# Kernel tuning notes

Measured on AMD Instinct MI355X. Metric: run time of the kernel, lower is better.

Reference implementation:

```python
import jax, jax.numpy as jnp
import numpy as np

N_NODES = 100000
N_EDGES = 1600000
D = 32
K = 3  # Chebyshev kernels
NEG_SLOPE = 0.2


def setup_inputs() -> dict:
    key = jax.random.key(0)
    ks = jax.random.split(key, 10)
    s = 1.0 / np.sqrt(D)
    return {
        "u": jax.random.normal(ks[0], (N_NODES, D), jnp.float32),
        "lambda_max": jnp.full((1,), 2.0, jnp.float32),
        "edge_src": jax.random.randint(ks[1], (N_EDGES,), 0, N_NODES, jnp.int32),
        "edge_dst": jax.random.randint(ks[2], (N_EDGES,), 0, N_NODES, jnp.int32),
        "cheb_W": jax.random.normal(ks[3], (K * D, D), jnp.float32) * s,
        "cheb_b": jnp.zeros((D,), jnp.float32),
        "src_W": jax.random.normal(ks[4], (D, D), jnp.float32) * s,
        "src_b": jnp.zeros((D,), jnp.float32),
        "dst_W": jax.random.normal(ks[5], (D, D), jnp.float32) * s,
        "dst_b": jnp.zeros((D,), jnp.float32),
        "attn": jax.random.normal(ks[6], (1, D), jnp.float32) * s,  # (heads=1, D)
    }


def reference(u, lambda_max, edge_src, edge_dst, cheb_W, cheb_b,
              src_W, src_b, dst_W, dst_b, attn):
    N = u.shape[0]
    # in-degrees (DGL: clamp(min=1) ** -0.5)
    deg = jnp.zeros((N,), u.dtype).at[edge_dst].add(1.0)
    Dinv = jnp.clip(deg, 1.0, None) ** -0.5  # (N,)

    def unnL(x):  # D^{-1/2} A D^{-1/2} x  via copy_u->sum message passing
        m = (x * Dinv[:, None])[edge_src]                       # (E, D)
        agg = jax.ops.segment_sum(m, edge_dst, num_segments=N)  # (N, D)
        return agg * Dinv[:, None]

    # --- ChebConv ---
    re_norm = 2.0 / lambda_max  # (1,) broadcast over all nodes
    X0 = u
    Xt = [X0]
    X1 = X0
    if K > 1:
        h = unnL(X0)
        X1 = -re_norm * h + X0 * (re_norm - 1.0)
        Xt.append(X1)
    for _ in range(2, K):
        h = unnL(X1)
        Xi = -2.0 * re_norm * h + X1 * (2.0 * (re_norm - 1.0)) - X0
        Xt.append(Xi)
        X0, X1 = X1, Xi
    Xcat = jnp.concatenate(Xt, axis=1)                 # (N, K*D)
    hc = jax.nn.relu(Xcat @ cheb_W + cheb_b)           # (N, D), DGL default activation=relu

    # --- GATv2Conv (heads=1) ---
    H = attn.shape[0]
    fsrc = (hc @ src_W + src_b).reshape(N, H, -1)      # (N, H, D)
    fdst = (hc @ dst_W + dst_b).reshape(N, H, -1)
    e = jax.nn.leaky_relu(fsrc[edge_src] + fdst[edge_dst], NEG_SLOPE)  # (E, H, D)
    logits = jnp.einsum('ehd,hd->eh', e, attn)         # (E, H)
    mx = jax.ops.segment_max(logits, edge_dst, num_segments=N)
    mx = jnp.where(jnp.isfinite(mx), mx, 0.0)
    ex = jnp.exp(logits - mx[edge_dst])
    den = jax.ops.segment_sum(ex, edge_dst, num_segments=N)
    a = ex / jnp.where(den > 0, den, 1.0)[edge_dst]    # edge softmax over dst groups
    msg = fsrc[edge_src] * a[:, :, None]               # (E, H, D)
    out = jax.ops.segment_sum(msg, edge_dst, num_segments=N)  # (N, H, D)
    return out.squeeze(1)
```

## Files before the change

kernel.cpp:

```cpp
#include <hip/hip_runtime.h>
#include <hip/hip_bf16.h>


typedef unsigned short u16;

#define DD 32
#define NEG_SLOPE 0.2f
#define BLK 256
#define TILE 4096
#define CB_SHIFT 8
#define CB_NODES 256
#define SRC_BITS 17

#define OFF_CHEBW 0
#define OFF_CHEBB 3072
#define OFF_SRCW  3104
#define OFF_SRCB  4128
#define OFF_DSTW  4160
#define OFF_DSTB  5184
#define OFF_ATTN  5216
#define OFF_LMAX  5248
#define W_TOTAL   5249

#define F_U     0
#define F_CHEBW 1
#define F_CHEBB 2
#define F_SRCW  3
#define F_SRCB  4
#define F_DSTW  5
#define F_DSTB  6
#define F_ATTN  7
#define F_LMAX  8
#define N_FLAGS 9

__device__ __forceinline__ float bh2f(u16 h) {
    return __uint_as_float(((unsigned)h) << 16);
}
__device__ __forceinline__ float rdin(const void* p, long long i, int f32f) {
    return f32f ? ((const float*)p)[i] : bh2f(((const u16*)p)[i]);
}
__device__ __forceinline__ float4 rd4(const void* p, long long row, int q, int f32f) {
    if (f32f) return ((const float4*)p)[row * 8 + q];
    ushort4 h = ((const ushort4*)p)[row * 8 + q];
    return make_float4(bh2f(h.x), bh2f(h.y), bh2f(h.z), bh2f(h.w));
}
__device__ __forceinline__ float lrelu(float x) { return fmaxf(x, NEG_SLOPE * x); }

__device__ __forceinline__ int plaus(u16 h) {
    if ((h & 0x7FFFu) == 0) return 1;
    unsigned e = (h >> 7) & 0xFF;
    return (e >= 0x60 && e <= 0x8F) ? 1 : 0;
}

template<int G>
__device__ __forceinline__ float4 bc8(float4 v) {
    constexpr int imm = (G << 5) | 0x18;
    float4 r;
    r.x = __int_as_float(__builtin_amdgcn_ds_swizzle(__float_as_int(v.x), imm));
    r.y = __int_as_float(__builtin_amdgcn_ds_swizzle(__float_as_int(v.y), imm));
    r.z = __int_as_float(__builtin_amdgcn_ds_swizzle(__float_as_int(v.z), imm));
    r.w = __int_as_float(__builtin_amdgcn_ds_swizzle(__float_as_int(v.w), imm));
    return r;
}

#define FMA4(ACC, S, W) \
    ACC.x = fmaf((S), (W).x, ACC.x); ACC.y = fmaf((S), (W).y, ACC.y); \
    ACC.z = fmaf((S), (W).z, ACC.z); ACC.w = fmaf((S), (W).w, ACC.w)

__global__ __launch_bounds__(BLK) void k_prep(
        const void* u, const void* chebW, const void* chebB, const void* srcW,
        const void* srcB, const void* dstW, const void* dstB, const void* attn,
        const void* lmax, int n0, int n7, int* __restrict__ flags,
        float* __restrict__ wsW, unsigned* __restrict__ Mabs,
        unsigned* __restrict__ gcnt) {
    __shared__ int cEven, cEvenZ, cOddNZ, fl;
    const void* ptrs[N_FLAGS] = {u, chebW, chebB, srcW, srcB, dstW, dstB, attn, lmax};
    const int   ns[N_FLAGS]   = {n0, 3072, 32, 1024, 32, 1024, 32, n7, 1};
    const int   offs[N_FLAGS] = {0, OFF_CHEBW, OFF_CHEBB, OFF_SRCW, OFF_SRCB,
                                 OFF_DSTW, OFF_DSTB, OFF_ATTN, OFF_LMAX};
    int a = blockIdx.x;
    if (a >= N_FLAGS) return;
    int t = threadIdx.x;
    const u16* h = (const u16*)ptrs[a];
    int n = ns[a];
    if (t == 0) { cEven = 0; cEvenZ = 0; cOddNZ = 0; }
    if (a == 0) {
        if (t < 32) Mabs[t] = 0u;
        if (t == 32) *gcnt = 0u;
    }
    __syncthreads();
    if (n == 1) {
        if (t == 0) {
            u16 v = h[0];
            fl = ((v & 0x7FFFu) == 0 || !plaus(v)) ? 1 : 0;
            flags[a] = fl;
        }
    } else {
        int nprobe = n >> 1;
        if (nprobe > 64) nprobe = 64;
        if (t < nprobe) {
            u16 ev = h[2 * t];
            u16 od = h[2 * t + 1];
            if (plaus(ev)) atomicAdd(&cEven, 1);
            if ((ev & 0x7FFFu) == 0) atomicAdd(&cEvenZ, 1);
            if (plaus(od) && (od & 0x7FFFu) != 0) atomicAdd(&cOddNZ, 1);
        }
        __syncthreads();
        if (t == 0) {
            int bf = (cEven * 4 >= nprobe * 3);
            if (cEvenZ == nprobe && cOddNZ * 2 >= nprobe) bf = 0;
            fl = bf ? 0 : 1;
            flags[a] = fl;
        }
    }
    __syncthreads();
    if (a == 0) return;
    int f = fl;
    int cnt = ns[a];
    int doff = offs[a];
    for (int i = t; i < cnt; i += BLK)
        wsW[doff + i] = rdin(ptrs[a], i, f);
}


__global__ __launch_bounds__(BLK) void k_h1(
        const int* __restrict__ dst, unsigned* __restrict__ hist1,
        int E, int T, int NB1) {
    __shared__ unsigned lh[512];
    int tile = blockIdx.x, t = threadIdx.x;
    for (int b = t; b < 512; b += BLK) lh[b] = 0;
    __syncthreads();
    int base = tile * TILE;
    for (int i = 0; i < TILE / BLK; i++) {
        int e = base + i * BLK + t;
        if (e < E) atomicAdd(&lh[dst[e] >> CB_SHIFT], 1u);
    }
    __syncthreads();
    for (int b = t; b < NB1; b += BLK) hist1[(size_t)b * T + tile] = lh[b];
}

__global__ __launch_bounds__(BLK) void k_scA(
        unsigned* __restrict__ h, unsigned* __restrict__ bsum, int T,
        unsigned* __restrict__ row_ptr, int N, int E,
        unsigned* __restrict__ gcnt) {
    __shared__ unsigned s[BLK];
    __shared__ int lastdone;
    int b = blockIdx.x, t = threadIdx.x;
    int NB = gridDim.x;
    unsigned carry = 0;
    for (int base = 0; base < T; base += BLK) {
        int i = base + t;
        unsigned v = (i < T) ? h[(size_t)b * T + i] : 0u;
        s[t] = v;
        __syncthreads();
        for (int off = 1; off < BLK; off <<= 1) {
            unsigned a = (t >= off) ? s[t - off] : 0u;
            __syncthreads();
            s[t] += a;
            __syncthreads();
        }
        if (i < T) h[(size_t)b * T + i] = carry + s[t] - v;
        carry += s[BLK - 1];
        __syncthreads();
    }
    if (t == 0) {
        bsum[b] = carry;
        __threadfence();
        unsigned old = atomicAdd(gcnt, 1u);
        lastdone = (old == (unsigned)(NB - 1)) ? 1 : 0;
    }
    __syncthreads();
    if (!lastdone) return;
    __threadfence();
    unsigned c2 = 0;
    for (int base = 0; base < NB; base += BLK) {
        int i = base + t;
        unsigned v = (i < NB) ? bsum[i] : 0u;
        s[t] = v;
        __syncthreads();
        for (int off = 1; off < BLK; off <<= 1) {
            unsigned a = (t >= off) ? s[t - off] : 0u;
            __syncthreads();
            s[t] += a;
            __syncthreads();
        }
        if (i < NB) bsum[i] = c2 + s[t] - v;
        c2 += s[BLK - 1];
        __syncthreads();
    }
    if (t == 0) row_ptr[N] = (unsigned)E;
}

__global__ __launch_bounds__(BLK) void k_s1(
        const int* __restrict__ src, const int* __restrict__ dst,
        const unsigned* __restrict__ off1, const unsigned* __restrict__ bsum,
        unsigned* __restrict__ tmp, int E, int T, int NB1) {
    __shared__ unsigned cur[512];
    int tile = blockIdx.x, t = threadIdx.x;
    for (int b = t; b < NB1; b += BLK)
        cur[b] = off1[(size_t)b * T + tile] + bsum[b];
    __syncthreads();
    int base = tile * TILE;
    for (int i = 0; i < TILE / BLK; i++) {
        int e = base + i * BLK + t;
        if (e < E) {
            int d = dst[e];
            unsigned pos = atomicAdd(&cur[d >> CB_SHIFT], 1u);
            tmp[pos] = ((unsigned)(d & (CB_NODES - 1)) << SRC_BITS) | (unsigned)src[e];
        }
    }
}

__global__ __launch_bounds__(BLK) void k_p2(
        const unsigned* __restrict__ tmp, const unsigned* __restrict__ bsum,
        unsigned* __restrict__ row_ptr, float* __restrict__ dinv,
        int* __restrict__ srcs, int N, int E, int T, int NB1) {
    __shared__ unsigned hist[CB_NODES], cur[CB_NODES], ssc[BLK];
    int b = blockIdx.x, t = threadIdx.x;
    int nodeBase = b << CB_SHIFT;
    unsigned lo = bsum[b];
    unsigned hi = (b + 1 < NB1) ? bsum[b + 1] : (unsigned)E;
    hist[t] = 0;
    __syncthreads();
    for (unsigned e = lo + t; e < hi; e += BLK)
        atomicAdd(&hist[tmp[e] >> SRC_BITS], 1u);
    __syncthreads();
    unsigned v = hist[t];
    ssc[t] = v;
    __syncthreads();
    for (int off = 1; off < BLK; off <<= 1) {
        unsigned a = (t >= off) ? ssc[t - off] : 0u;
        __syncthreads();
        ssc[t] += a;
        __syncthreads();
    }
    unsigned ex = ssc[t] - v;
    cur[t] = ex;
    int node = nodeBase + t;
    if (node < N) {
        row_ptr[node] = lo + ex;
        unsigned c = v;
        if (c < 1u) c = 1u;
        dinv[node] = rsqrtf((float)c);
    }
    __syncthreads();
    for (unsigned e = lo + t; e < hi; e += BLK) {
        unsigned p = tmp[e];
        unsigned pos = lo + atomicAdd(&cur[p >> SRC_BITS], 1u);
        srcs[pos] = (int)(p & ((1u << SRC_BITS) - 1u));
    }
}


__global__ __launch_bounds__(BLK) void k_unnl1(
        const void* __restrict__ u, const int* __restrict__ flags,
        const float* __restrict__ dinv, const unsigned* __restrict__ row_ptr,
        const int* __restrict__ srcs, const float* __restrict__ wsW,
        float* __restrict__ X1, int N) {
    int node = (blockIdx.x * BLK + threadIdx.x) >> 3;
    if (node >= N) return;
    int q = threadIdx.x & 7;
    int f = flags[F_U];
    int base = (int)row_ptr[node], end = (int)row_ptr[node + 1];
    float4 acc = make_float4(0.f, 0.f, 0.f, 0.f);
    for (int i = base; i < end; i += 4) {
        int e1 = i + 1, e2 = i + 2, e3 = i + 3;
        int s0 = srcs[i];
        int s1 = srcs[min(e1, end - 1)];
        int s2 = srcs[min(e2, end - 1)];
        int s3 = srcs[min(e3, end - 1)];
        float dv0 = dinv[s0], dv1 = dinv[s1], dv2 = dinv[s2], dv3 = dinv[s3];
        if (e1 >= end) dv1 = 0.f;
        if (e2 >= end) dv2 = 0.f;
        if (e3 >= end) dv3 = 0.f;
        float4 x0 = rd4(u, s0, q, f);
        float4 x1 = rd4(u, s1, q, f);
        float4 x2 = rd4(u, s2, q, f);
        float4 x3 = rd4(u, s3, q, f);
        acc.x += x0.x * dv0 + x1.x * dv1 + x2.x * dv2 + x3.x * dv3;
        acc.y += x0.y * dv0 + x1.y * dv1 + x2.y * dv2 + x3.y * dv3;
        acc.z += x0.z * dv0 + x1.z * dv1 + x2.z * dv2 + x3.z * dv3;
        acc.w += x0.w * dv0 + x1.w * dv1 + x2.w * dv2 + x3.w * dv3;
    }
    float rn = 2.0f / wsW[OFF_LMAX];
    float dn = dinv[node];
    float4 x0 = rd4(u, node, q, f);
    float4 r;
    r.x = -rn * (acc.x * dn) + x0.x * (rn - 1.f);
    r.y = -rn * (acc.y * dn) + x0.y * (rn - 1.f);
    r.z = -rn * (acc.z * dn) + x0.z * (rn - 1.f);
    r.w = -rn * (acc.w * dn) + x0.w * (rn - 1.f);
    ((float4*)X1)[(size_t)node * 8 + q] = r;
}

__global__ __launch_bounds__(BLK) void k_unnl2(
        const void* __restrict__ u, const int* __restrict__ flags,
        const float* __restrict__ X1, const float* __restrict__ dinv,
        const unsigned* __restrict__ row_ptr, const int* __restrict__ srcs,
        const float* __restrict__ wsW, float* __restrict__ X2, int N) {
    int node = (blockIdx.x * BLK + threadIdx.x) >> 3;
    if (node >= N) return;
    int q = threadIdx.x & 7;
    int base = (int)row_ptr[node], end = (int)row_ptr[node + 1];
    float4 acc = make_float4(0.f, 0.f, 0.f, 0.f);
    for (int i = base; i < end; i += 4) {
        int e1 = i + 1, e2 = i + 2, e3 = i + 3;
        int s0 = srcs[i];
        int s1 = srcs[min(e1, end - 1)];
        int s2 = srcs[min(e2, end - 1)];
        int s3 = srcs[min(e3, end - 1)];
        float dv0 = dinv[s0], dv1 = dinv[s1], dv2 = dinv[s2], dv3 = dinv[s3];
        if (e1 >= end) dv1 = 0.f;
        if (e2 >= end) dv2 = 0.f;
        if (e3 >= end) dv3 = 0.f;
        float4 x0 = ((const float4*)X1)[(size_t)s0 * 8 + q];
        float4 x1 = ((const float4*)X1)[(size_t)s1 * 8 + q];
        float4 x2 = ((const float4*)X1)[(size_t)s2 * 8 + q];
        float4 x3 = ((const float4*)X1)[(size_t)s3 * 8 + q];
        acc.x += x0.x * dv0 + x1.x * dv1 + x2.x * dv2 + x3.x * dv3;
        acc.y += x0.y * dv0 + x1.y * dv1 + x2.y * dv2 + x3.y * dv3;
        acc.z += x0.z * dv0 + x1.z * dv1 + x2.z * dv2 + x3.z * dv3;
        acc.w += x0.w * dv0 + x1.w * dv1 + x2.w * dv2 + x3.w * dv3;
    }
    float rn = 2.0f / wsW[OFF_LMAX];
    float dn = dinv[node];
    float4 x0 = rd4(u, node, q, flags[F_U]);
    float4 x1 = ((const float4*)X1)[(size_t)node * 8 + q];
    float4 r;
    r.x = -2.f * rn * (acc.x * dn) + x1.x * (2.f * (rn - 1.f)) - x0.x;
    r.y = -2.f * rn * (acc.y * dn) + x1.y * (2.f * (rn - 1.f)) - x0.y;
    r.z = -2.f * rn * (acc.z * dn) + x1.z * (2.f * (rn - 1.f)) - x0.z;
    r.w = -2.f * rn * (acc.w * dn) + x1.w * (2.f * (rn - 1.f)) - x0.w;
    ((float4*)X2)[(size_t)node * 8 + q] = r;
}

__global__ __launch_bounds__(BLK, 4) void k_cfsd(
        const void* __restrict__ u, const int* __restrict__ flags,
        const float* __restrict__ X1, const float* __restrict__ X2,
        const float* __restrict__ wsW, float* __restrict__ fsrc,
        float* __restrict__ fdst, unsigned* __restrict__ Mabs, int N) {
    __shared__ __align__(16) float sW[3072], sWs[1024], sWd[1024];
    __shared__ __align__(16) float sb[32], sbs[32], sbd[32];
    __shared__ unsigned mloc[32];
    int t = threadIdx.x;
    for (int i = t; i < 3072; i += BLK) sW[i] = wsW[OFF_CHEBW + i];
    for (int i = t; i < 1024; i += BLK) {
        sWs[i] = wsW[OFF_SRCW + i];
        sWd[i] = wsW[OFF_DSTW + i];
    }
    if (t < 32) {
        sb[t]  = wsW[OFF_CHEBB + t];
        sbs[t] = wsW[OFF_SRCB + t];
        sbd[t] = wsW[OFF_DSTB + t];
        mloc[t] = 0u;
    }
    __syncthreads();
    int f = flags[F_U];
    int q = t & 7;
    long long node = (long long)((blockIdx.x * BLK + t) >> 3);
    bool valid = node < N;
    long long row = valid ? node : (N - 1);

    const float4* fW = (const float4*)sW;
    float4 acc = ((const float4*)sb)[q];

#define CHEB_STEP(XQ, B4, I4) { \
    float4 xv = bc8<I4>(XQ); \
    const float4* wp = fW + (B4) + (I4) * 32 + q; \
    float4 w; \
    w = wp[0];  FMA4(acc, xv.x, w); \
    w = wp[8];  FMA4(acc, xv.y, w); \
    w = wp[16]; FMA4(acc, xv.z, w); \
    w = wp[24]; FMA4(acc, xv.w, w); }
#define CHEB8(XQ, B4) \
    CHEB_STEP(XQ, B4, 0) CHEB_STEP(XQ, B4, 1) CHEB_STEP(XQ, B4, 2) \
    CHEB_STEP(XQ, B4, 3) CHEB_STEP(XQ, B4, 4) CHEB_STEP(XQ, B4, 5) \
    CHEB_STEP(XQ, B4, 6) CHEB_STEP(XQ, B4, 7)

    {
        float4 xq = rd4(u, row, q, f);
        CHEB8(xq, 0)
    }
    {
        float4 xq = ((const float4*)X1)[row * 8 + q];
        CHEB8(xq, 256)
    }
    {
        float4 xq = ((const float4*)X2)[row * 8 + q];
        CHEB8(xq, 512)
    }
#undef CHEB8
#undef CHEB_STEP

    acc.x = fmaxf(acc.x, 0.f); acc.y = fmaxf(acc.y, 0.f);
    acc.z = fmaxf(acc.z, 0.f); acc.w = fmaxf(acc.w, 0.f);

    const float4* fWs = (const float4*)sWs;
    const float4* fWd = (const float4*)sWd;
    float4 as = ((const float4*)sbs)[q];
    float4 ad = ((const float4*)sbd)[q];
#define PROJ_G(G) { \
    float4 h = bc8<G>(acc); \
    const float4* wsp = fWs + (4 * (G)) * 8 + q; \
    const float4* wdp = fWd + (4 * (G)) * 8 + q; \
    float4 w; \
    w = wsp[0];  FMA4(as, h.x, w); \
    w = wsp[8];  FMA4(as, h.y, w); \
    w = wsp[16]; FMA4(as, h.z, w); \
    w = wsp[24]; FMA4(as, h.w, w); \
    w = wdp[0];  FMA4(ad, h.x, w); \
    w = wdp[8];  FMA4(ad, h.y, w); \
    w = wdp[16]; FMA4(ad, h.z, w); \
    w = wdp[24]; FMA4(ad, h.w, w); }
    PROJ_G(0) PROJ_G(1) PROJ_G(2) PROJ_G(3)
    PROJ_G(4) PROJ_G(5) PROJ_G(6) PROJ_G(7)
#undef PROJ_G

    float mabs = 0.f;
    if (valid) {
        ((float4*)fsrc)[row * 8 + q] = as;
        ((float4*)fdst)[row * 8 + q] = ad;
        mabs = fmaxf(fmaxf(fabsf(as.x), fabsf(as.y)),
                     fmaxf(fabsf(as.z), fabsf(as.w)));
    }
    atomicMax(&mloc[t & 31], __float_as_uint(mabs));
    __syncthreads();
    if (t < 32) atomicMax(&Mabs[t], mloc[t]);
}

__global__ __launch_bounds__(BLK) void k_gat(
        const float* __restrict__ fsrc, const float* __restrict__ fdst,
        const unsigned* __restrict__ row_ptr, const int* __restrict__ srcs,
        const float* __restrict__ wsW, const unsigned* __restrict__ Mabs,
        float* __restrict__ out, int N) {
    int node = (blockIdx.x * BLK + threadIdx.x) >> 3;
    if (node >= N) return;
    int q = threadIdx.x & 7;
    int base = (int)row_ptr[node], end = (int)row_ptr[node + 1];
    if (base == end) {
        ((float4*)out)[(size_t)node * 8 + q] = make_float4(0.f, 0.f, 0.f, 0.f);
        return;
    }
    float4 fd = ((const float4*)fdst)[(size_t)node * 8 + q];
    float4 at = ((const float4*)(wsW + OFF_ATTN))[q];
    float4 mb = ((const float4*)Mabs)[q];
    float kp = (mb.x + fabsf(fd.x)) * fabsf(at.x) +
               (mb.y + fabsf(fd.y)) * fabsf(at.y) +
               (mb.z + fabsf(fd.z)) * fabsf(at.z) +
               (mb.w + fabsf(fd.w)) * fabsf(at.w);
    kp += __shfl_xor(kp, 1);
    kp += __shfl_xor(kp, 2);
    kp += __shfl_xor(kp, 4);
    float K = kp;
    float4 acc = make_float4(0.f, 0.f, 0.f, 0.f);
    float den = 0.f;
    for (int i = base; i < end; i += 2) {
        int e1 = i + 1;
        int s0 = srcs[i];
        int s1 = srcs[min(e1, end - 1)];
        float4 fs0 = ((const float4*)fsrc)[(size_t)s0 * 8 + q];
        float4 fs1 = ((const float4*)fsrc)[(size_t)s1 * 8 + q];
        float v0 = lrelu(fs0.x + fd.x) * at.x + lrelu(fs0.y + fd.y) * at.y +
                   lrelu(fs0.z + fd.z) * at.z + lrelu(fs0.w + fd.w) * at.w;
        float v1 = lrelu(fs1.x + fd.x) * at.x + lrelu(fs1.y + fd.y) * at.y +
                   lrelu(fs1.z + fd.z) * at.z + lrelu(fs1.w + fd.w) * at.w;
        v0 += __shfl_xor(v0, 1);  v1 += __shfl_xor(v1, 1);
        v0 += __shfl_xor(v0, 2);  v1 += __shfl_xor(v1, 2);
        v0 += __shfl_xor(v0, 4);  v1 += __shfl_xor(v1, 4);
        float w0 = __expf(v0 - K);
        float w1 = (e1 < end) ? __expf(v1 - K) : 0.f;
        acc.x += fs0.x * w0 + fs1.x * w1;
        acc.y += fs0.y * w0 + fs1.y * w1;
        acc.z += fs0.z * w0 + fs1.z * w1;
        acc.w += fs0.w * w0 + fs1.w * w1;
        den += w0 + w1;
    }
    float inv = 1.f / (den > 0.f ? den : 1.f);
    ((float4*)out)[(size_t)node * 8 + q] =
        make_float4(acc.x * inv, acc.y * inv, acc.z * inv, acc.w * inv);
}

extern "C" void kernel_launch(void* const* d_in, const int* in_sizes, int n_in,
                              void* d_out, int out_size, void* d_ws, size_t ws_size,
                              hipStream_t stream) {
    const void* u     = d_in[0];
    const void* lmax  = d_in[1];
    const int*  esrc  = (const int*)d_in[2];
    const int*  edst  = (const int*)d_in[3];
    const void* chebW = d_in[4];
    const void* chebB = d_in[5];
    const void* srcW  = d_in[6];
    const void* srcB  = d_in[7];
    const void* dstW  = d_in[8];
    const void* dstB  = d_in[9];
    const void* attn  = d_in[10];

    const int ND = in_sizes[0];
    const int N  = ND / DD;
    const int E  = in_sizes[2];

    const int NB1 = (N + CB_NODES - 1) >> CB_SHIFT;
    const int T   = (E + TILE - 1) / TILE;
    const int M   = NB1 * T;

    float* ws   = (float*)d_ws;
    float* X1   = ws;
    float* X2   = ws + (size_t)ND;
    unsigned* tmp = (unsigned*)(ws + 2 * (size_t)ND);
    int*   srcs = (int*)(tmp + E);
    unsigned* hist1   = (unsigned*)(srcs + E);
    unsigned* row_ptr = hist1 + M;
    float*    dinv    = (float*)(row_ptr + (N + 1));
    unsigned* bsum    = (unsigned*)(dinv + N);
    float*    wsW     = (float*)(((uintptr_t)(bsum + NB1) + 15) & ~(uintptr_t)15);
    int*      flags   = (int*)(wsW + W_TOTAL);
    unsigned* Mabs    = (unsigned*)(((uintptr_t)(flags + N_FLAGS) + 15) & ~(uintptr_t)15);
    unsigned* gcnt    = Mabs + 32;
    float*    out     = (float*)d_out;

    auto gb = [](long long n, int b) { return (unsigned)((n + b - 1) / b); };

    k_prep<<<N_FLAGS, BLK, 0, stream>>>(u, chebW, chebB, srcW, srcB, dstW, dstB,
                                        attn, lmax, ND, DD, flags, wsW, Mabs, gcnt);

    k_h1<<<T, BLK, 0, stream>>>(edst, hist1, E, T, NB1);
    k_scA<<<NB1, BLK, 0, stream>>>(hist1, bsum, T, row_ptr, N, E, gcnt);
    k_s1<<<T, BLK, 0, stream>>>(esrc, edst, hist1, bsum, tmp, E, T, NB1);
    k_p2<<<NB1, BLK, 0, stream>>>(tmp, bsum, row_ptr, dinv, srcs, N, E, T, NB1);

    k_unnl1<<<gb((long long)N * 8, BLK), BLK, 0, stream>>>(u, flags, dinv, row_ptr,
                                                           srcs, wsW, X1, N);
    k_unnl2<<<gb((long long)N * 8, BLK), BLK, 0, stream>>>(u, flags, X1, dinv, row_ptr,
                                                           srcs, wsW, X2, N);

    k_cfsd<<<gb((long long)N * 8, BLK), BLK, 0, stream>>>(u, flags, X1, X2, wsW,
                                                          X1, X2, Mabs, N);

    k_gat<<<gb((long long)N * 8, BLK), BLK, 0, stream>>>(X1, X2, row_ptr, srcs,
                                                         wsW, Mabs, out, N);
}
```

Before: 299.0 us.

## Fuse second Chebyshev propagation with dense projection kernel, stage fdst in output

The second Laplacian propagation is merged into the Chebyshev matmul and GAT projection kernel, so X2 is never written to or reread from global memory and one launch disappears. Weights are now read straight from global memory (cached) instead of being staged in LDS, which removes the per-block weight load and syncthreads. fdst is written into the output buffer, which k_gat reads and overwrites in place, so restrict is dropped there. The cost is higher register pressure and a gather-heavy loop sharing a kernel with the dense math, which may lower occupancy, and the invalid tail threads now run the gather on a clamped node.

```diff
diff --git a/kernel.cpp b/kernel.cpp
--- a/kernel.cpp
+++ b/kernel.cpp
@@ -293,14 +293,21 @@
     ((float4*)X1)[(size_t)node * 8 + q] = r;
 }
 
-__global__ __launch_bounds__(BLK) void k_unnl2(
+__global__ __launch_bounds__(BLK, 4) void k_unnl2f(
         const void* __restrict__ u, const int* __restrict__ flags,
         const float* __restrict__ X1, const float* __restrict__ dinv,
         const unsigned* __restrict__ row_ptr, const int* __restrict__ srcs,
-        const float* __restrict__ wsW, float* __restrict__ X2, int N) {
-    int node = (blockIdx.x * BLK + threadIdx.x) >> 3;
-    if (node >= N) return;
-    int q = threadIdx.x & 7;
+        const float* __restrict__ wsW, float* __restrict__ fsrc,
+        float* __restrict__ fdst, unsigned* __restrict__ Mabs, int N) {
+    __shared__ unsigned mloc[32];
+    int t = threadIdx.x;
+    if (t < 32) mloc[t] = 0u;
+    __syncthreads();
+    int node0 = (blockIdx.x * BLK + t) >> 3;
+    bool valid = node0 < N;
+    long long node = valid ? (long long)node0 : (long long)(N - 1);
+    int q = t & 7;
+    int f = flags[F_U];
     int base = (int)row_ptr[node], end = (int)row_ptr[node + 1];
     float4 acc = make_float4(0.f, 0.f, 0.f, 0.f);
     for (int i = base; i < end; i += 4) {
@@ -324,83 +331,42 @@
     }
     float rn = 2.0f / wsW[OFF_LMAX];
     float dn = dinv[node];
-    float4 x0 = rd4(u, node, q, flags[F_U]);
-    float4 x1 = ((const float4*)X1)[(size_t)node * 8 + q];
-    float4 r;
-    r.x = -2.f * rn * (acc.x * dn) + x1.x * (2.f * (rn - 1.f)) - x0.x;
-    r.y = -2.f * rn * (acc.y * dn) + x1.y * (2.f * (rn - 1.f)) - x0.y;
-    r.z = -2.f * rn * (acc.z * dn) + x1.z * (2.f * (rn - 1.f)) - x0.z;
-    r.w = -2.f * rn * (acc.w * dn) + x1.w * (2.f * (rn - 1.f)) - x0.w;
-    ((float4*)X2)[(size_t)node * 8 + q] = r;
-}
-
-__global__ __launch_bounds__(BLK, 4) void k_cfsd(
-        const void* __restrict__ u, const int* __restrict__ flags,
-        const float* __restrict__ X1, const float* __restrict__ X2,
-        const float* __restrict__ wsW, float* __restrict__ fsrc,
-        float* __restrict__ fdst, unsigned* __restrict__ Mabs, int N) {
-    __shared__ __align__(16) float sW[3072], sWs[1024], sWd[1024];
-    __shared__ __align__(16) float sb[32], sbs[32], sbd[32];
-    __shared__ unsigned mloc[32];
-    int t = threadIdx.x;
-    for (int i = t; i < 3072; i += BLK) sW[i] = wsW[OFF_CHEBW + i];
-    for (int i = t; i < 1024; i += BLK) {
-        sWs[i] = wsW[OFF_SRCW + i];
-        sWd[i] = wsW[OFF_DSTW + i];
-    }
-    if (t < 32) {
-        sb[t]  = wsW[OFF_CHEBB + t];
-        sbs[t] = wsW[OFF_SRCB + t];
-        sbd[t] = wsW[OFF_DSTB + t];
-        mloc[t] = 0u;
-    }
-    __syncthreads();
-    int f = flags[F_U];
-    int q = t & 7;
-    long long node = (long long)((blockIdx.x * BLK + t) >> 3);
-    bool valid = node < N;
-    long long row = valid ? node : (N - 1);
-
-    const float4* fW = (const float4*)sW;
-    float4 acc = ((const float4*)sb)[q];
-
+    float4 xu = rd4(u, node, q, f);
+    float4 xc1 = ((const float4*)X1)[node * 8 + q];
+    float4 xc2;
+    xc2.x = -2.f * rn * (acc.x * dn) + xc1.x * (2.f * (rn - 1.f)) - xu.x;
+    xc2.y = -2.f * rn * (acc.y * dn) + xc1.y * (2.f * (rn - 1.f)) - xu.y;
+    xc2.z = -2.f * rn * (acc.z * dn) + xc1.z * (2.f * (rn - 1.f)) - xu.z;
+    xc2.w = -2.f * rn * (acc.w * dn) + xc1.w * (2.f * (rn - 1.f)) - xu.w;
+
+    const float4* fW = (const float4*)(wsW + OFF_CHEBW);
+    float4 hc = ((const float4*)(wsW + OFF_CHEBB))[q];
 #define CHEB_STEP(XQ, B4, I4) { \
     float4 xv = bc8<I4>(XQ); \
     const float4* wp = fW + (B4) + (I4) * 32 + q; \
     float4 w; \
-    w = wp[0];  FMA4(acc, xv.x, w); \
-    w = wp[8];  FMA4(acc, xv.y, w); \
-    w = wp[16]; FMA4(acc, xv.z, w); \
-    w = wp[24]; FMA4(acc, xv.w, w); }
+    w = wp[0];  FMA4(hc, xv.x, w); \
+    w = wp[8];  FMA4(hc, xv.y, w); \
+    w = wp[16]; FMA4(hc, xv.z, w); \
+    w = wp[24]; FMA4(hc, xv.w, w); }
 #define CHEB8(XQ, B4) \
     CHEB_STEP(XQ, B4, 0) CHEB_STEP(XQ, B4, 1) CHEB_STEP(XQ, B4, 2) \
     CHEB_STEP(XQ, B4, 3) CHEB_STEP(XQ, B4, 4) CHEB_STEP(XQ, B4, 5) \
     CHEB_STEP(XQ, B4, 6) CHEB_STEP(XQ, B4, 7)
-
-    {
-        float4 xq = rd4(u, row, q, f);
-        CHEB8(xq, 0)
-    }
-    {
-        float4 xq = ((const float4*)X1)[row * 8 + q];
-        CHEB8(xq, 256)
-    }
-    {
-        float4 xq = ((const float4*)X2)[row * 8 + q];
-        CHEB8(xq, 512)
-    }
+    CHEB8(xu, 0)
+    CHEB8(xc1, 256)
+    CHEB8(xc2, 512)
 #undef CHEB8
 #undef CHEB_STEP
-
-    acc.x = fmaxf(acc.x, 0.f); acc.y = fmaxf(acc.y, 0.f);
-    acc.z = fmaxf(acc.z, 0.f); acc.w = fmaxf(acc.w, 0.f);
-
-    const float4* fWs = (const float4*)sWs;
-    const float4* fWd = (const float4*)sWd;
-    float4 as = ((const float4*)sbs)[q];
-    float4 ad = ((const float4*)sbd)[q];
+    hc.x = fmaxf(hc.x, 0.f); hc.y = fmaxf(hc.y, 0.f);
+    hc.z = fmaxf(hc.z, 0.f); hc.w = fmaxf(hc.w, 0.f);
+
+    const float4* fWs = (const float4*)(wsW + OFF_SRCW);
+    const float4* fWd = (const float4*)(wsW + OFF_DSTW);
+    float4 as = ((const float4*)(wsW + OFF_SRCB))[q];
+    float4 ad = ((const float4*)(wsW + OFF_DSTB))[q];
 #define PROJ_G(G) { \
-    float4 h = bc8<G>(acc); \
+    float4 h = bc8<G>(hc); \
     const float4* wsp = fWs + (4 * (G)) * 8 + q; \
     const float4* wdp = fWd + (4 * (G)) * 8 + q; \
     float4 w; \
@@ -418,8 +384,8 @@
 
     float mabs = 0.f;
     if (valid) {
-        ((float4*)fsrc)[row * 8 + q] = as;
-        ((float4*)fdst)[row * 8 + q] = ad;
+        ((float4*)fsrc)[node * 8 + q] = as;
+        ((float4*)fdst)[node * 8 + q] = ad;
         mabs = fmaxf(fmaxf(fabsf(as.x), fabsf(as.y)),
                      fmaxf(fabsf(as.z), fabsf(as.w)));
     }
@@ -429,10 +395,10 @@
 }
 
 __global__ __launch_bounds__(BLK) void k_gat(
-        const float* __restrict__ fsrc, const float* __restrict__ fdst,
+        const float* __restrict__ fsrc, const float* fdst,
         const unsigned* __restrict__ row_ptr, const int* __restrict__ srcs,
         const float* __restrict__ wsW, const unsigned* __restrict__ Mabs,
-        float* __restrict__ out, int N) {
+        float* out, int N) {
     int node = (blockIdx.x * BLK + threadIdx.x) >> 3;
     if (node >= N) return;
     int q = threadIdx.x & 7;
@@ -505,7 +471,7 @@
 
     float* ws   = (float*)d_ws;
     float* X1   = ws;
-    float* X2   = ws + (size_t)ND;
+    float* F1   = ws + (size_t)ND;
     unsigned* tmp = (unsigned*)(ws + 2 * (size_t)ND);
     int*   srcs = (int*)(tmp + E);
     unsigned* hist1   = (unsigned*)(srcs + E);
@@ -530,12 +496,10 @@
 
     k_unnl1<<<gb((long long)N * 8, BLK), BLK, 0, stream>>>(u, flags, dinv, row_ptr,
                                                            srcs, wsW, X1, N);
-    k_unnl2<<<gb((long long)N * 8, BLK), BLK, 0, stream>>>(u, flags, X1, dinv, row_ptr,
-                                                           srcs, wsW, X2, N);
-
-    k_cfsd<<<gb((long long)N * 8, BLK), BLK, 0, stream>>>(u, flags, X1, X2, wsW,
-                                                          X1, X2, Mabs, N);
-
-    k_gat<<<gb((long long)N * 8, BLK), BLK, 0, stream>>>(X1, X2, row_ptr, srcs,
+    k_unnl2f<<<gb((long long)N * 8, BLK), BLK, 0, stream>>>(u, flags, X1, dinv,
+                                                            row_ptr, srcs, wsW,
+                                                            F1, out, Mabs, N);
+
+    k_gat<<<gb((long long)N * 8, BLK), BLK, 0, stream>>>(F1, out, row_ptr, srcs,
                                                          wsW, Mabs, out, N);
 }
```

Result: no change. 303.4 us (+1.5%).
